# Kernel tuning notes

Hardware: AMD Instinct MI355X
Metric: run time of the kernel (lower is better)

The kernel has to match this reference:

```python
import jax, jax.numpy as jnp
import numpy as np

B, S, C = 8, 1024, 1280   # B = 2*N (uncond|cond halves), S = 32*32 latent tokens
H, D = 20, 64             # heads, head_dim; H*D == C


def setup_inputs() -> dict:
    key = jax.random.key(0)
    ks = jax.random.split(key, 5)
    std = 1.0 / np.sqrt(C)
    return {
        "hidden_states": jax.random.normal(ks[0], (B, S, C), jnp.float32),
        "Wq": jax.random.normal(ks[1], (C, C), jnp.float32) * std,
        "Wk": jax.random.normal(ks[2], (C, C), jnp.float32) * std,
        "Wv": jax.random.normal(ks[3], (C, C), jnp.float32) * std,
        "Wo": jax.random.normal(ks[4], (C, C), jnp.float32) * std,
        "bo": jnp.zeros((C,), jnp.float32),
    }


def _inject(x, n):
    # replicate reference rows 0 (uncond) and n (cond) across each half
    unc = jnp.broadcast_to(x[0:1], (n,) + x.shape[1:])
    con = jnp.broadcast_to(x[n:n + 1], (n,) + x.shape[1:])
    return jnp.concatenate([unc, con], axis=0)


def reference(hidden_states, Wq, Wk, Wv, Wo, bo):
    b, s, c = hidden_states.shape
    n = b // 2
    q = hidden_states @ Wq
    k = hidden_states @ Wk
    v = hidden_states @ Wv
    # PnP injection (self-attention, share_enabled, n > 1, all injections on)
    q = _inject(q, n)
    k = _inject(k, n)
    v = _inject(v, n)
    # head split: [b, s, c] -> [b, h, s, d]
    q = q.reshape(b, s, H, D).transpose(0, 2, 1, 3)
    k = k.reshape(b, s, H, D).transpose(0, 2, 1, 3)
    v = v.reshape(b, s, H, D).transpose(0, 2, 1, 3)
    scale = 1.0 / np.sqrt(D)
    scores = jnp.einsum("bhqd,bhkd->bhqk", q, k) * scale
    probs = jax.nn.softmax(scores, axis=-1)
    out = jnp.einsum("bhqk,bhkd->bhqd", probs, v)
    out = out.transpose(0, 2, 1, 3).reshape(b, s, c)
    return out @ Wo + bo
```

## Files before the change

### kernel.cpp

```cpp
#include <hip/hip_runtime.h>

#define S_LEN 1024
#define C_DIM 1280
#define NH 20
#define HD 64

typedef __attribute__((ext_vector_type(8))) short short8;
typedef __attribute__((ext_vector_type(4))) short short4v;
typedef __attribute__((ext_vector_type(4))) float float4v;

__device__ __forceinline__ float bf2f(unsigned short u) {
    union { unsigned u; float f; } v; v.u = ((unsigned)u) << 16; return v.f;
}
__device__ __forceinline__ unsigned short f2bf(float f) {
    union { float f; unsigned u; } v; v.f = f;
    unsigned u = v.u;
    return (unsigned short)((u + 0x7FFFu + ((u >> 16) & 1u)) >> 16);
}

__device__ __forceinline__ void load_lds16(const unsigned short* g, unsigned short* l) {
    __builtin_amdgcn_global_load_lds(
        (const __attribute__((address_space(1))) unsigned int*)g,
        (__attribute__((address_space(3))) unsigned int*)l, 16, 0, 0);
}

__global__ __launch_bounds__(256) void detect_kernel(
    const unsigned int* __restrict__ w, int* __restrict__ flag)
{
    __shared__ int cnt;
    if (threadIdx.x == 0) cnt = 0;
    __syncthreads();
    int local = 0;
    for (int i = threadIdx.x; i < 1024; i += 256) {
        unsigned e = (w[i] >> 7) & 0xFFu;
        if (e >= 100u && e <= 140u) local++;
    }
    atomicAdd(&cnt, local);
    __syncthreads();
    if (threadIdx.x == 0) *flag = (cnt < 512) ? 1 : 0;
}

__global__ __launch_bounds__(256) void convx_kernel(
    const void* __restrict__ hs, const int* __restrict__ flag,
    unsigned short* __restrict__ X)
{
    const size_t SC = (size_t)S_LEN * C_DIM;
    int g = blockIdx.y;
    size_t off = ((size_t)blockIdx.x * 256 + threadIdx.x) * 8;
    size_t src = (size_t)g * 4 * SC + off;
    short8 o;
    if (*flag) {
        const float* p = (const float*)hs + src;
        for (int j = 0; j < 8; j++) o[j] = (short)f2bf(p[j]);
    } else {
        o = *(const short8*)((const unsigned short*)hs + src);
    }
    *(short8*)(X + g * SC + off) = o;
}

__global__ __launch_bounds__(256) void convw_kernel(
    const void* __restrict__ Wq, const void* __restrict__ Wk,
    const void* __restrict__ Wv, const void* __restrict__ Wo,
    const int* __restrict__ flag, unsigned short* __restrict__ WT)
{
    __shared__ unsigned short tile[64 * 68];
    const void* W = (blockIdx.z == 0) ? Wq : (blockIdx.z == 1) ? Wk
                    : (blockIdx.z == 2) ? Wv : Wo;
    unsigned short* T = WT + (size_t)blockIdx.z * C_DIM * C_DIM;
    int fp32 = *flag;
    int c0 = blockIdx.x * 64, r0 = blockIdx.y * 64;
    int t = threadIdx.x;
    int r = t >> 3, cg = t & 7;
    for (int rep = 0; rep < 2; rep++) {
        int rr = r0 + r + rep * 32;
        if (fp32) {
            const float* p = (const float*)W + (size_t)rr * C_DIM + c0 + cg * 8;
            for (int j = 0; j < 8; j++)
                tile[(r + rep * 32) * 68 + cg * 8 + j] = f2bf(p[j]);
        } else {
            short8 v = *(const short8*)((const unsigned short*)W + (size_t)rr * C_DIM + c0 + cg * 8);
            for (int j = 0; j < 8; j++)
                tile[(r + rep * 32) * 68 + cg * 8 + j] = (unsigned short)v[j];
        }
    }
    __syncthreads();
    int c = t >> 3, rg = t & 7;
    for (int rep = 0; rep < 2; rep++) {
        short8 o;
        for (int j = 0; j < 8; j++)
            o[j] = (short)tile[(rg * 8 + j) * 68 + c + rep * 32];
        *(short8*)(T + (size_t)(c0 + c + rep * 32) * C_DIM + r0 + rg * 8) = o;
    }
}

__global__ __launch_bounds__(256) void gemm_qkv_kernel(
    const unsigned short* __restrict__ X,
    const unsigned short* __restrict__ WT,
    unsigned short* __restrict__ Qo, unsigned short* __restrict__ Ko,
    unsigned short* __restrict__ Vt)
{
    __shared__ unsigned short Alds[128 * 72];
    int z = blockIdx.z;
    const unsigned short* Wt = WT + (size_t)z * C_DIM * C_DIM;
    int c0 = blockIdx.x * 128, r0 = blockIdx.y * 128;
    int t = threadIdx.x, wave = t >> 6, lane = t & 63;
    int wr = wave >> 1, wc = wave & 1, quad = lane >> 4, mn = lane & 15;
    int g = r0 >> 10;
    const unsigned short* xb = X + (size_t)r0 * C_DIM;
    float4v acc[4][4] = {};
    for (int k0 = 0; k0 < C_DIM; k0 += 64) {
        for (int rep = 0; rep < 4; rep++) {
            int chunk = rep * 256 + t;
            int r = chunk >> 3, kg = chunk & 7;
            short8 v = *(const short8*)(xb + (size_t)r * C_DIM + k0 + kg * 8);
            *(short8*)(&Alds[r * 72 + kg * 8]) = v;
        }
        __syncthreads();
        for (int kc = 0; kc < 2; kc++) {
            short8 a[4], b[4];
            for (int mt = 0; mt < 4; mt++)
                a[mt] = *(const short8*)(&Alds[(wr * 64 + mt * 16 + mn) * 72 + kc * 32 + quad * 8]);
            for (int nt = 0; nt < 4; nt++)
                b[nt] = *(const short8*)(Wt + (size_t)(c0 + wc * 64 + nt * 16 + mn) * C_DIM
                                            + k0 + kc * 32 + quad * 8);
            for (int mt = 0; mt < 4; mt++)
                for (int nt = 0; nt < 4; nt++)
                    acc[mt][nt] = __builtin_amdgcn_mfma_f32_16x16x32_bf16(a[mt], b[nt], acc[mt][nt], 0, 0, 0);
        }
        __syncthreads();
    }
    if (z == 2) {
        for (int mt = 0; mt < 4; mt++) {
            int row = r0 + wr * 64 + mt * 16 + quad * 4;
            int s = row & 1023;
            for (int nt = 0; nt < 4; nt++) {
                int col = c0 + wc * 64 + nt * 16 + mn;
                short4v p;
                for (int i = 0; i < 4; i++) p[i] = (short)f2bf(acc[mt][nt][i]);
                *(short4v*)(Vt + ((size_t)g * C_DIM + col) * S_LEN + s) = p;
            }
        }
    } else {
        unsigned short* Out = (z == 0) ? Qo : Ko;
        for (int mt = 0; mt < 4; mt++) {
            int row = r0 + wr * 64 + mt * 16 + quad * 4;
            for (int nt = 0; nt < 4; nt++) {
                int col = c0 + wc * 64 + nt * 16 + mn;
                for (int i = 0; i < 4; i++)
                    Out[(size_t)(row + i) * C_DIM + col] = f2bf(acc[mt][nt][i]);
            }
        }
    }
}

__global__ __launch_bounds__(256) void attn_kernel(
    const unsigned short* __restrict__ Q, const unsigned short* __restrict__ K,
    const unsigned short* __restrict__ VT, unsigned short* __restrict__ O)
{
    __shared__ unsigned short Kl[2][64 * 64];
    __shared__ unsigned short Vl[2][64 * 64];
    __shared__ unsigned short Pl[4 * 16 * 72];
    int qt = blockIdx.x, h = blockIdx.y, g = blockIdx.z;
    int t = threadIdx.x, wave = t >> 6, lane = t & 63;
    int quad = lane >> 4, n = lane & 15;
    const size_t SC = (size_t)S_LEN * C_DIM;
    const unsigned short* Qb = Q + (size_t)g * SC;
    const unsigned short* Kb = K + (size_t)g * SC + h * HD;
    const unsigned short* Vb = VT + (size_t)g * SC + (size_t)(h * HD) * S_LEN;
    unsigned short* Pw = &Pl[wave * 16 * 72];

    int srow = wave * 8 + (lane >> 3);
    int slot = lane & 7;

    short8 qa[2];
    int qrow = qt * 64 + wave * 16 + n;
    for (int kc = 0; kc < 2; kc++) {
        short8 v = *(const short8*)(Qb + (size_t)qrow * C_DIM + h * HD + kc * 32 + quad * 8);
        short8 w;
        for (int j = 0; j < 8; j++)
            w[j] = (short)f2bf(bf2f((unsigned short)v[j]) * 0.125f);
        qa[kc] = w;
    }

    for (int p = 0; p < 2; p++) {
        int row = p * 32 + srow;
        int ck = slot ^ (row & 7);
        load_lds16(Kb + (size_t)row * C_DIM + ck * 8, &Kl[0][row * 64 + slot * 8]);
        load_lds16(Vb + (size_t)row * S_LEN + ck * 8, &Vl[0][row * 64 + slot * 8]);
    }
    asm volatile("s_waitcnt vmcnt(0)" ::: "memory");
    __builtin_amdgcn_s_barrier();

    float4v oacc[4] = {};
    float lsum[4] = { 0.f, 0.f, 0.f, 0.f };

    for (int kt = 0; kt < 16; kt++) {
        int cur = kt & 1, nxt = cur ^ 1;
        if (kt < 15) {
            for (int p = 0; p < 2; p++) {
                int row = p * 32 + srow;
                int ck = slot ^ (row & 7);
                load_lds16(Kb + (size_t)((kt + 1) * 64 + row) * C_DIM + ck * 8,
                           &Kl[nxt][row * 64 + slot * 8]);
                load_lds16(Vb + (size_t)row * S_LEN + (kt + 1) * 64 + ck * 8,
                           &Vl[nxt][row * 64 + slot * 8]);
            }
        }
        const unsigned short* Kt = Kl[cur];
        const unsigned short* Vt = Vl[cur];

        float4v sacc[4] = {};
        for (int kc = 0; kc < 2; kc++)
            for (int nt = 0; nt < 4; nt++) {
                int row = nt * 16 + n;
                short8 kb = *(const short8*)(Kt + row * 64 + (((kc * 4 + quad) ^ (row & 7)) * 8));
                sacc[nt] = __builtin_amdgcn_mfma_f32_16x16x32_bf16(qa[kc], kb, sacc[nt], 0, 0, 0);
            }

        for (int nt = 0; nt < 4; nt++)
            for (int i = 0; i < 4; i++) {
                float p = __expf(sacc[nt][i]);
                lsum[i] += p;
                Pw[(quad * 4 + i) * 72 + nt * 16 + n] = f2bf(p);
            }
        asm volatile("s_waitcnt lgkmcnt(0)" ::: "memory");
        short8 pa0 = *(const short8*)(&Pw[n * 72 + quad * 8]);
        short8 pa1 = *(const short8*)(&Pw[n * 72 + 32 + quad * 8]);
        for (int kc = 0; kc < 2; kc++) {
            short8 pa = kc ? pa1 : pa0;
            for (int nt = 0; nt < 4; nt++) {
                int row = nt * 16 + n;
                short8 vb = *(const short8*)(Vt + row * 64 + (((kc * 4 + quad) ^ (row & 7)) * 8));
                oacc[nt] = __builtin_amdgcn_mfma_f32_16x16x32_bf16(pa, vb, oacc[nt], 0, 0, 0);
            }
        }
        asm volatile("s_waitcnt vmcnt(0)" ::: "memory");
        __builtin_amdgcn_s_barrier();
    }

    for (int i = 0; i < 4; i++)
        for (int d = 1; d < 16; d <<= 1)
            lsum[i] += __shfl_xor(lsum[i], d, 64);
    float inv[4];
    for (int i = 0; i < 4; i++) inv[i] = 1.0f / lsum[i];

    int row0 = qt * 64 + wave * 16 + quad * 4;
    for (int nt = 0; nt < 4; nt++)
        for (int i = 0; i < 4; i++)
            O[(size_t)g * SC + (size_t)(row0 + i) * C_DIM + h * HD + nt * 16 + n] =
                f2bf(oacc[nt][i] * inv[i]);
}

__global__ __launch_bounds__(256) void gemm_out_kernel(
    const unsigned short* __restrict__ X,
    const unsigned short* __restrict__ WoT,
    const void* __restrict__ bo,
    const int* __restrict__ flag,
    void* __restrict__ out)
{
    __shared__ unsigned short Alds[128 * 72];
    int c0 = blockIdx.x * 128, r0 = blockIdx.y * 128;
    int t = threadIdx.x, wave = t >> 6, lane = t & 63;
    int wr = wave >> 1, wc = wave & 1, quad = lane >> 4, mn = lane & 15;
    const unsigned short* xb = X + (size_t)r0 * C_DIM;
    int fp32 = *flag;
    float4v acc[4][4] = {};
    for (int k0 = 0; k0 < C_DIM; k0 += 64) {
        for (int rep = 0; rep < 4; rep++) {
            int chunk = rep * 256 + t;
            int r = chunk >> 3, kg = chunk & 7;
            short8 v = *(const short8*)(xb + (size_t)r * C_DIM + k0 + kg * 8);
            *(short8*)(&Alds[r * 72 + kg * 8]) = v;
        }
        __syncthreads();
        for (int kc = 0; kc < 2; kc++) {
            short8 a[4], b[4];
            for (int mt = 0; mt < 4; mt++)
                a[mt] = *(const short8*)(&Alds[(wr * 64 + mt * 16 + mn) * 72 + kc * 32 + quad * 8]);
            for (int nt = 0; nt < 4; nt++)
                b[nt] = *(const short8*)(WoT + (size_t)(c0 + wc * 64 + nt * 16 + mn) * C_DIM
                                             + k0 + kc * 32 + quad * 8);
            for (int mt = 0; mt < 4; mt++)
                for (int nt = 0; nt < 4; nt++)
                    acc[mt][nt] = __builtin_amdgcn_mfma_f32_16x16x32_bf16(a[mt], b[nt], acc[mt][nt], 0, 0, 0);
        }
        __syncthreads();
    }
    for (int mt = 0; mt < 4; mt++) {
        int row = r0 + wr * 64 + mt * 16 + quad * 4;
        int g = row >> 10;
        for (int nt = 0; nt < 4; nt++) {
            int col = c0 + wc * 64 + nt * 16 + mn;
            float bb = fp32 ? ((const float*)bo)[col] : bf2f(((const unsigned short*)bo)[col]);
            for (int i = 0; i < 4; i++) {
                float v = acc[mt][nt][i] + bb;
                int s = (row + i) & 1023;
                if (fp32) {
                    float* o = (float*)out;
                    for (int rep = 0; rep < 4; rep++)
                        o[((size_t)(g * 4 + rep) * S_LEN + s) * C_DIM + col] = v;
                } else {
                    unsigned short* o = (unsigned short*)out;
                    unsigned short bv = f2bf(v);
                    for (int rep = 0; rep < 4; rep++)
                        o[((size_t)(g * 4 + rep) * S_LEN + s) * C_DIM + col] = bv;
                }
            }
        }
    }
}

extern "C" void kernel_launch(void* const* d_in, const int* in_sizes, int n_in,
                              void* d_out, int out_size, void* d_ws, size_t ws_size,
                              hipStream_t stream)
{
    const void* hs = d_in[0];
    const void* Wq = d_in[1];
    const void* Wk = d_in[2];
    const void* Wv = d_in[3];
    const void* Wo = d_in[4];
    const void* bo = d_in[5];

    const size_t CC  = (size_t)C_DIM * C_DIM;
    const size_t SC2 = (size_t)2 * S_LEN * C_DIM;

    int* flag = (int*)d_ws;
    unsigned short* base = (unsigned short*)((char*)d_ws + 256);
    unsigned short* WT = base;
    unsigned short* X  = WT + 4 * CC;
    unsigned short* Q  = X + SC2;
    unsigned short* K  = Q + SC2;
    unsigned short* VT = K + SC2;

    hipLaunchKernelGGL(detect_kernel, dim3(1), dim3(256), 0, stream,
                       (const unsigned int*)Wq, flag);
    hipLaunchKernelGGL(convx_kernel, dim3(640, 2), dim3(256), 0, stream,
                       hs, flag, X);
    hipLaunchKernelGGL(convw_kernel, dim3(20, 20, 4), dim3(256), 0, stream,
                       Wq, Wk, Wv, Wo, flag, WT);
    hipLaunchKernelGGL(gemm_qkv_kernel, dim3(10, 16, 3), dim3(256), 0, stream,
                       X, WT, Q, K, VT);
    hipLaunchKernelGGL(attn_kernel, dim3(16, NH, 2), dim3(256), 0, stream,
                       Q, K, VT, X );
    hipLaunchKernelGGL(gemm_out_kernel, dim3(10, 16), dim3(256), 0, stream,
                       X, WT + 3 * CC, bo, flag, d_out);
}
```

Measured before the change: 249.5 us.

## Double-buffer GEMM tiles in LDS via async global_load_lds with XOR swizzle

Rewrites the QKV and output projection GEMMs to stage both A and B tiles in LDS using global_load_lds, double-buffered so the next k-tile loads while the current one feeds MFMA. It adds an XOR swizzle on the LDS layout to avoid bank conflicts and shrinks tiles (64x128 for QKV, 64x64 for the output GEMM) so more blocks fill the CUs. Before this, B operands were read straight from global memory in the inner loop. The smaller tiles lower per-block arithmetic intensity, and each k-step still ends with a full vmcnt wait plus barrier.

```diff
diff --git a/kernel.cpp b/kernel.cpp
--- a/kernel.cpp
+++ b/kernel.cpp
@@ -99,42 +99,67 @@
     unsigned short* __restrict__ Qo, unsigned short* __restrict__ Ko,
     unsigned short* __restrict__ Vt)
 {
-    __shared__ unsigned short Alds[128 * 72];
+    __shared__ __align__(16) unsigned short Al[2][64 * 64];
+    __shared__ __align__(16) unsigned short Bl[2][128 * 64];
     int z = blockIdx.z;
     const unsigned short* Wt = WT + (size_t)z * C_DIM * C_DIM;
-    int c0 = blockIdx.x * 128, r0 = blockIdx.y * 128;
+    int c0 = blockIdx.x * 128, r0 = blockIdx.y * 64;
     int t = threadIdx.x, wave = t >> 6, lane = t & 63;
-    int wr = wave >> 1, wc = wave & 1, quad = lane >> 4, mn = lane & 15;
-    int g = r0 >> 10;
+    int quad = lane >> 4, mn = lane & 15;
+    int srow = wave * 8 + (lane >> 3), slot = lane & 7;
     const unsigned short* xb = X + (size_t)r0 * C_DIM;
-    float4v acc[4][4] = {};
-    for (int k0 = 0; k0 < C_DIM; k0 += 64) {
-        for (int rep = 0; rep < 4; rep++) {
-            int chunk = rep * 256 + t;
-            int r = chunk >> 3, kg = chunk & 7;
-            short8 v = *(const short8*)(xb + (size_t)r * C_DIM + k0 + kg * 8);
-            *(short8*)(&Alds[r * 72 + kg * 8]) = v;
-        }
-        __syncthreads();
+    const unsigned short* wb = Wt + (size_t)c0 * C_DIM;
+
+    for (int p = 0; p < 2; p++) {
+        int row = p * 32 + srow; int ck = slot ^ (row & 7);
+        load_lds16(xb + (size_t)row * C_DIM + ck * 8, &Al[0][row * 64 + slot * 8]);
+    }
+    for (int p = 0; p < 4; p++) {
+        int row = p * 32 + srow; int ck = slot ^ (row & 7);
+        load_lds16(wb + (size_t)row * C_DIM + ck * 8, &Bl[0][row * 64 + slot * 8]);
+    }
+    asm volatile("s_waitcnt vmcnt(0)" ::: "memory");
+    __builtin_amdgcn_s_barrier();
+
+    float4v acc[4][2] = {};
+    for (int kt = 0; kt < 20; kt++) {
+        int cur = kt & 1, nxt = cur ^ 1;
+        if (kt < 19) {
+            int k0 = (kt + 1) * 64;
+            for (int p = 0; p < 2; p++) {
+                int row = p * 32 + srow; int ck = slot ^ (row & 7);
+                load_lds16(xb + (size_t)row * C_DIM + k0 + ck * 8, &Al[nxt][row * 64 + slot * 8]);
+            }
+            for (int p = 0; p < 4; p++) {
+                int row = p * 32 + srow; int ck = slot ^ (row & 7);
+                load_lds16(wb + (size_t)row * C_DIM + k0 + ck * 8, &Bl[nxt][row * 64 + slot * 8]);
+            }
+        }
         for (int kc = 0; kc < 2; kc++) {
-            short8 a[4], b[4];
+            short8 a[4], b[2];
+            for (int mt = 0; mt < 4; mt++) {
+                int row = mt * 16 + mn;
+                a[mt] = *(const short8*)(&Al[cur][row * 64 + (((kc * 4 + quad) ^ (row & 7)) * 8)]);
+            }
+            for (int nt = 0; nt < 2; nt++) {
+                int row = wave * 32 + nt * 16 + mn;
+                b[nt] = *(const short8*)(&Bl[cur][row * 64 + (((kc * 4 + quad) ^ (row & 7)) * 8)]);
+            }
             for (int mt = 0; mt < 4; mt++)
-                a[mt] = *(const short8*)(&Alds[(wr * 64 + mt * 16 + mn) * 72 + kc * 32 + quad * 8]);
-            for (int nt = 0; nt < 4; nt++)
-                b[nt] = *(const short8*)(Wt + (size_t)(c0 + wc * 64 + nt * 16 + mn) * C_DIM
-                                            + k0 + kc * 32 + quad * 8);
-            for (int mt = 0; mt < 4; mt++)
-                for (int nt = 0; nt < 4; nt++)
+                for (int nt = 0; nt < 2; nt++)
                     acc[mt][nt] = __builtin_amdgcn_mfma_f32_16x16x32_bf16(a[mt], b[nt], acc[mt][nt], 0, 0, 0);
         }
-        __syncthreads();
-    }
+        asm volatile("s_waitcnt vmcnt(0)" ::: "memory");
+        __builtin_amdgcn_s_barrier();
+    }
+
     if (z == 2) {
+        int g = r0 >> 10;
         for (int mt = 0; mt < 4; mt++) {
-            int row = r0 + wr * 64 + mt * 16 + quad * 4;
+            int row = r0 + mt * 16 + quad * 4;
             int s = row & 1023;
-            for (int nt = 0; nt < 4; nt++) {
-                int col = c0 + wc * 64 + nt * 16 + mn;
+            for (int nt = 0; nt < 2; nt++) {
+                int col = c0 + wave * 32 + nt * 16 + mn;
                 short4v p;
                 for (int i = 0; i < 4; i++) p[i] = (short)f2bf(acc[mt][nt][i]);
                 *(short4v*)(Vt + ((size_t)g * C_DIM + col) * S_LEN + s) = p;
@@ -143,9 +168,9 @@
     } else {
         unsigned short* Out = (z == 0) ? Qo : Ko;
         for (int mt = 0; mt < 4; mt++) {
-            int row = r0 + wr * 64 + mt * 16 + quad * 4;
-            for (int nt = 0; nt < 4; nt++) {
-                int col = c0 + wc * 64 + nt * 16 + mn;
+            int row = r0 + mt * 16 + quad * 4;
+            for (int nt = 0; nt < 2; nt++) {
+                int col = c0 + wave * 32 + nt * 16 + mn;
                 for (int i = 0; i < 4; i++)
                     Out[(size_t)(row + i) * C_DIM + col] = f2bf(acc[mt][nt][i]);
             }
@@ -157,8 +182,8 @@
     const unsigned short* __restrict__ Q, const unsigned short* __restrict__ K,
     const unsigned short* __restrict__ VT, unsigned short* __restrict__ O)
 {
-    __shared__ unsigned short Kl[2][64 * 64];
-    __shared__ unsigned short Vl[2][64 * 64];
+    __shared__ __align__(16) unsigned short Kl[2][64 * 64];
+    __shared__ __align__(16) unsigned short Vl[2][64 * 64];
     __shared__ unsigned short Pl[4 * 16 * 72];
     int qt = blockIdx.x, h = blockIdx.y, g = blockIdx.z;
     int t = threadIdx.x, wave = t >> 6, lane = t & 63;
@@ -258,39 +283,58 @@
     const int* __restrict__ flag,
     void* __restrict__ out)
 {
-    __shared__ unsigned short Alds[128 * 72];
-    int c0 = blockIdx.x * 128, r0 = blockIdx.y * 128;
+    __shared__ __align__(16) unsigned short Al[2][64 * 64];
+    __shared__ __align__(16) unsigned short Bl[2][64 * 64];
+    int c0 = blockIdx.x * 64, r0 = blockIdx.y * 64;
     int t = threadIdx.x, wave = t >> 6, lane = t & 63;
     int wr = wave >> 1, wc = wave & 1, quad = lane >> 4, mn = lane & 15;
+    int srow = wave * 8 + (lane >> 3), slot = lane & 7;
     const unsigned short* xb = X + (size_t)r0 * C_DIM;
+    const unsigned short* wb = WoT + (size_t)c0 * C_DIM;
     int fp32 = *flag;
-    float4v acc[4][4] = {};
-    for (int k0 = 0; k0 < C_DIM; k0 += 64) {
-        for (int rep = 0; rep < 4; rep++) {
-            int chunk = rep * 256 + t;
-            int r = chunk >> 3, kg = chunk & 7;
-            short8 v = *(const short8*)(xb + (size_t)r * C_DIM + k0 + kg * 8);
-            *(short8*)(&Alds[r * 72 + kg * 8]) = v;
-        }
-        __syncthreads();
+
+    for (int p = 0; p < 2; p++) {
+        int row = p * 32 + srow; int ck = slot ^ (row & 7);
+        load_lds16(xb + (size_t)row * C_DIM + ck * 8, &Al[0][row * 64 + slot * 8]);
+        load_lds16(wb + (size_t)row * C_DIM + ck * 8, &Bl[0][row * 64 + slot * 8]);
+    }
+    asm volatile("s_waitcnt vmcnt(0)" ::: "memory");
+    __builtin_amdgcn_s_barrier();
+
+    float4v acc[2][2] = {};
+    for (int kt = 0; kt < 20; kt++) {
+        int cur = kt & 1, nxt = cur ^ 1;
+        if (kt < 19) {
+            int k0 = (kt + 1) * 64;
+            for (int p = 0; p < 2; p++) {
+                int row = p * 32 + srow; int ck = slot ^ (row & 7);
+                load_lds16(xb + (size_t)row * C_DIM + k0 + ck * 8, &Al[nxt][row * 64 + slot * 8]);
+                load_lds16(wb + (size_t)row * C_DIM + k0 + ck * 8, &Bl[nxt][row * 64 + slot * 8]);
+            }
+        }
         for (int kc = 0; kc < 2; kc++) {
-            short8 a[4], b[4];
-            for (int mt = 0; mt < 4; mt++)
-                a[mt] = *(const short8*)(&Alds[(wr * 64 + mt * 16 + mn) * 72 + kc * 32 + quad * 8]);
-            for (int nt = 0; nt < 4; nt++)
-                b[nt] = *(const short8*)(WoT + (size_t)(c0 + wc * 64 + nt * 16 + mn) * C_DIM
-                                             + k0 + kc * 32 + quad * 8);
-            for (int mt = 0; mt < 4; mt++)
-                for (int nt = 0; nt < 4; nt++)
+            short8 a[2], b[2];
+            for (int mt = 0; mt < 2; mt++) {
+                int row = wr * 32 + mt * 16 + mn;
+                a[mt] = *(const short8*)(&Al[cur][row * 64 + (((kc * 4 + quad) ^ (row & 7)) * 8)]);
+            }
+            for (int nt = 0; nt < 2; nt++) {
+                int row = wc * 32 + nt * 16 + mn;
+                b[nt] = *(const short8*)(&Bl[cur][row * 64 + (((kc * 4 + quad) ^ (row & 7)) * 8)]);
+            }
+            for (int mt = 0; mt < 2; mt++)
+                for (int nt = 0; nt < 2; nt++)
                     acc[mt][nt] = __builtin_amdgcn_mfma_f32_16x16x32_bf16(a[mt], b[nt], acc[mt][nt], 0, 0, 0);
         }
-        __syncthreads();
-    }
-    for (int mt = 0; mt < 4; mt++) {
-        int row = r0 + wr * 64 + mt * 16 + quad * 4;
+        asm volatile("s_waitcnt vmcnt(0)" ::: "memory");
+        __builtin_amdgcn_s_barrier();
+    }
+
+    for (int mt = 0; mt < 2; mt++) {
+        int row = r0 + wr * 32 + mt * 16 + quad * 4;
         int g = row >> 10;
-        for (int nt = 0; nt < 4; nt++) {
-            int col = c0 + wc * 64 + nt * 16 + mn;
+        for (int nt = 0; nt < 2; nt++) {
+            int col = c0 + wc * 32 + nt * 16 + mn;
             float bb = fp32 ? ((const float*)bo)[col] : bf2f(((const unsigned short*)bo)[col]);
             for (int i = 0; i < 4; i++) {
                 float v = acc[mt][nt][i] + bb;
@@ -338,10 +382,10 @@
                        hs, flag, X);
     hipLaunchKernelGGL(convw_kernel, dim3(20, 20, 4), dim3(256), 0, stream,
                        Wq, Wk, Wv, Wo, flag, WT);
-    hipLaunchKernelGGL(gemm_qkv_kernel, dim3(10, 16, 3), dim3(256), 0, stream,
+    hipLaunchKernelGGL(gemm_qkv_kernel, dim3(10, 32, 3), dim3(256), 0, stream,
                        X, WT, Q, K, VT);
     hipLaunchKernelGGL(attn_kernel, dim3(16, NH, 2), dim3(256), 0, stream,
                        Q, K, VT, X );
-    hipLaunchKernelGGL(gemm_out_kernel, dim3(10, 16), dim3(256), 0, stream,
+    hipLaunchKernelGGL(gemm_out_kernel, dim3(20, 32), dim3(256), 0, stream,
                        X, WT + 3 * CC, bo, flag, d_out);
 }
```

Measured after the change: 219.8 us. 1.14x faster.
